# Optimization experiments

Hardware: AMD Instinct MI355X
Metric: run time of the kernel (lower is better)

The kernel has to match this reference:

```python
import jax, jax.numpy as jnp
import numpy as np

N_NODES = 100000


def setup_inputs() -> dict:
    key = jax.random.key(0)
    k1, k2, k3, k4, k5, k6 = jax.random.split(key, 6)
    N, E, DIN, DOUT = N_NODES, 1600000, 64, 64
    feature = jax.random.normal(k1, (N, DIN), dtype=jnp.float32)
    norm = jax.random.uniform(k2, (N, 1), dtype=jnp.float32)  # per-node 1/sqrt(deg)-style norm
    src = jax.random.randint(k3, (E,), 0, N, dtype=jnp.int32)
    dst = jax.random.randint(k4, (E,), 0, N, dtype=jnp.int32)
    W = jax.random.normal(k5, (DOUT, DIN), dtype=jnp.float32) / jnp.sqrt(jnp.float32(DIN))
    b = jax.random.normal(k6, (DOUT,), dtype=jnp.float32)
    return {"feature": feature, "norm": norm, "src": src, "dst": dst, "W": W, "b": b}


def reference(feature, norm, src, dst, W, b):
    # message: h_src * norm_src, gathered per edge -> [E, DIN]
    msg = (feature * norm)[src]
    # reduce: scatter-sum over destination nodes, then renormalize by dst norm
    accum = jax.ops.segment_sum(msg, dst, num_segments=N_NODES) * norm  # [N, DIN]
    # final Linear: accum @ W^T + b
    return accum @ W.T + b
```

## Files before the change

### kernel.cpp

```cpp
#include <hip/hip_runtime.h>
#include <hip/hip_bf16.h>

#define N_NODES 100000
#define D 64
#define BNODES 128
#define NBKT 782
#define SCAP 16
#define BCAP 4608
#define CAP 48
#define SENT 0xFFFFFFFFu

__global__ __launch_bounds__(256) void pre_linear_kernel(
    const float* __restrict__ feature,
    const float* __restrict__ norm,
    const float* __restrict__ W,
    __hip_bfloat16* __restrict__ Zb,
    int* __restrict__ bkt_cnt)
{
    __shared__ float Wt[D * 65];
    __shared__ float accsm[4][D];

    int gid = blockIdx.x * blockDim.x + threadIdx.x;
    if (gid < NBKT) bkt_cnt[gid] = 0;

    for (int i = threadIdx.x; i < D * D; i += blockDim.x) {
        int o = i >> 6, k = i & 63;
        Wt[k * 65 + o] = W[o * D + k];
    }
    __syncthreads();

    const int lane = threadIdx.x & 63;
    const int wid  = threadIdx.x >> 6;

    float wreg[D];
    #pragma unroll
    for (int k = 0; k < D; ++k) wreg[k] = Wt[k * 65 + lane];
    float* const mysm = &accsm[wid][0];

    const int wave   = gid >> 6;
    const int nwaves = gridDim.x * (blockDim.x >> 6);

    for (int node = wave; node < N_NODES; node += nwaves) {
        float x = feature[node * D + lane] * norm[node];
        mysm[lane] = x;
        __builtin_amdgcn_wave_barrier();
        float r = 0.f;
        #pragma unroll
        for (int j = 0; j < D / 4; ++j) {
            float4 a4 = *(const float4*)&mysm[j * 4];
            r = fmaf(a4.x, wreg[4 * j + 0], r);
            r = fmaf(a4.y, wreg[4 * j + 1], r);
            r = fmaf(a4.z, wreg[4 * j + 2], r);
            r = fmaf(a4.w, wreg[4 * j + 3], r);
        }
        Zb[node * D + lane] = __float2bfloat16(r);
        __builtin_amdgcn_wave_barrier();
    }
}

__global__ __launch_bounds__(1024) void bin_scatter_kernel(
    const int* __restrict__ src, const int* __restrict__ dst,
    int* __restrict__ bkt_cnt,
    unsigned int* __restrict__ barr,
    int E)
{
    __shared__ unsigned int stage[NBKT][SCAP];
    __shared__ int scnt[NBKT];

    for (int i = threadIdx.x; i < NBKT; i += blockDim.x) scnt[i] = 0;
    __syncthreads();

    const int nthreads = gridDim.x * blockDim.x;
    for (int e = blockIdx.x * blockDim.x + threadIdx.x; e < E; e += nthreads) {
        int t = dst[e];
        int b = t >> 7;
        unsigned u = ((unsigned)src[e] << 7) | (unsigned)(t & 127);
        int slot = atomicAdd(&scnt[b], 1);
        if (slot < SCAP) {
            stage[b][slot] = u;
        } else {
            int g = atomicAdd(&bkt_cnt[b], 16);
            if (g + 16 <= BCAP) {
                unsigned int* dp = barr + (size_t)b * BCAP + g;
                dp[0] = u;
                #pragma unroll
                for (int k = 1; k < 16; ++k) dp[k] = SENT;
            }
        }
    }
    __syncthreads();

    for (int bb = threadIdx.x; bb < NBKT; bb += blockDim.x) {
        int n_live = scnt[bb];
        if (n_live > SCAP) n_live = SCAP;
        if (n_live > 0) {
            int g = atomicAdd(&bkt_cnt[bb], 16);
            if (g + 16 <= BCAP) {
                unsigned int* dp = barr + (size_t)bb * BCAP + g;
                for (int k = 0; k < n_live; ++k) dp[k] = stage[bb][k];
                for (int k = n_live; k < 16; ++k) dp[k] = SENT;
            }
        }
    }
}

__device__ inline float2 bf2f(unsigned int z) {
    float2 r;
    r.x = __uint_as_float(z << 16);
    r.y = __uint_as_float(z & 0xffff0000u);
    return r;
}

__global__ __launch_bounds__(512) void csr_gather_kernel(
    const __hip_bfloat16* __restrict__ Zb,
    const float* __restrict__ norm,
    const int* __restrict__ bkt_cnt,
    const unsigned int* __restrict__ barr,
    const float* __restrict__ bias,
    float* __restrict__ out)
{
    __shared__ int slab[BNODES * CAP];
    __shared__ int lcnt[BNODES];

    const int b   = blockIdx.x;
    const int tid = threadIdx.x;

    for (int i = tid; i < BNODES; i += blockDim.x) lcnt[i] = 0;
    __syncthreads();

    int n = bkt_cnt[b];
    if (n > BCAP) n = BCAP;
    const unsigned int* bp = barr + (size_t)b * BCAP;
    for (int i = tid * 4; i < n; i += blockDim.x * 4) {
        uint4 u4 = *(const uint4*)&bp[i];
        unsigned us[4] = {u4.x, u4.y, u4.z, u4.w};
        #pragma unroll
        for (int j = 0; j < 4; ++j) {
            unsigned u = us[j];
            if (u != SENT) {
                int local = (int)(u & 127);
                int pos = atomicAdd(&lcnt[local], 1);
                if (pos < CAP) slab[local * CAP + pos] = (int)(u >> 7);
            }
        }
    }
    __syncthreads();

    const int lane = tid & 63;
    const int wid  = tid >> 6;
    const int q    = lane >> 4;
    const int c    = lane & 15;

    const float4 bi = *(const float4*)&bias[4 * c];

    for (int nl = wid; nl < BNODES; nl += 8) {
        int node = (b << 7) + nl;
        if (node >= N_NODES) continue;

        int len = lcnt[nl];
        if (len > CAP) len = CAP;
        const int* sl = &slab[nl * CAP];

        float ax = 0.f, ay = 0.f, az = 0.f, aw = 0.f;
        int i = 0;
        for (; i + 16 <= len; i += 16) {
            int s0 = sl[i + 0  + q];
            int s1 = sl[i + 4  + q];
            int s2 = sl[i + 8  + q];
            int s3 = sl[i + 12 + q];
            uint2 z0 = *(const uint2*)&Zb[s0 * D + 4 * c];
            uint2 z1 = *(const uint2*)&Zb[s1 * D + 4 * c];
            uint2 z2 = *(const uint2*)&Zb[s2 * D + 4 * c];
            uint2 z3 = *(const uint2*)&Zb[s3 * D + 4 * c];
            float2 a0 = bf2f(z0.x), b0 = bf2f(z0.y);
            float2 a1 = bf2f(z1.x), b1 = bf2f(z1.y);
            float2 a2 = bf2f(z2.x), b2 = bf2f(z2.y);
            float2 a3 = bf2f(z3.x), b3 = bf2f(z3.y);
            ax += a0.x + a1.x + a2.x + a3.x;
            ay += a0.y + a1.y + a2.y + a3.y;
            az += b0.x + b1.x + b2.x + b3.x;
            aw += b0.y + b1.y + b2.y + b3.y;
        }
        for (; i < len; i += 4) {
            int idx = i + q;
            if (idx < len) {
                int s = sl[idx];
                uint2 z = *(const uint2*)&Zb[s * D + 4 * c];
                float2 a = bf2f(z.x), bb2 = bf2f(z.y);
                ax += a.x; ay += a.y; az += bb2.x; aw += bb2.y;
            }
        }

        ax += __shfl(ax, lane ^ 16, 64);
        ay += __shfl(ay, lane ^ 16, 64);
        az += __shfl(az, lane ^ 16, 64);
        aw += __shfl(aw, lane ^ 16, 64);
        ax += __shfl(ax, lane ^ 32, 64);
        ay += __shfl(ay, lane ^ 32, 64);
        az += __shfl(az, lane ^ 32, 64);
        aw += __shfl(aw, lane ^ 32, 64);

        if (q == 0) {
            float nv = norm[node];
            float4 o;
            o.x = fmaf(nv, ax, bi.x);
            o.y = fmaf(nv, ay, bi.y);
            o.z = fmaf(nv, az, bi.z);
            o.w = fmaf(nv, aw, bi.w);
            *(float4*)&out[node * D + 4 * c] = o;
        }
    }
}

extern "C" void kernel_launch(void* const* d_in, const int* in_sizes, int n_in,
                              void* d_out, int out_size, void* d_ws, size_t ws_size,
                              hipStream_t stream)
{
    const float* feature = (const float*)d_in[0];
    const float* norm    = (const float*)d_in[1];
    const int*   src     = (const int*)d_in[2];
    const int*   dst     = (const int*)d_in[3];
    const float* W       = (const float*)d_in[4];
    const float* b       = (const float*)d_in[5];
    float*       out     = (float*)d_out;

    const int E = in_sizes[2];

    char* p = (char*)d_ws;
    __hip_bfloat16* Zb      = (__hip_bfloat16*)p;  p += (size_t)N_NODES * D * 2;
    unsigned int*   barr    = (unsigned int*)p;    p += (size_t)NBKT * BCAP * 4;
    int*            bkt_cnt = (int*)p;

    pre_linear_kernel<<<3125, 256, 0, stream>>>(feature, norm, W, Zb, bkt_cnt);

    bin_scatter_kernel<<<256, 1024, 0, stream>>>(src, dst, bkt_cnt, barr, E);

    csr_gather_kernel<<<NBKT, 512, 0, stream>>>(Zb, norm, bkt_cnt, barr, b, out);
}
```

Baseline: 169.3 us.

## Use fixed per-block bucket slots to drop global atomics in bin flush

Each of the 256 scatter blocks now writes its 16-entry staged chunk for every bucket into a fixed slot indexed by block and bucket, using vectorized uint4 stores from four threads per bucket. This removes the global atomicAdd on bkt_cnt during the flush phase; only overflow entries still go through atomics into a separate overflow region. The gather kernel reads all 256 fixed chunks per bucket plus the overflow region. In exchange it always writes and reads full sentinel-padded chunks even for empty buckets, which raises memory traffic and spreads each bucket's reads across strided addresses.

Result: faster. 159.7 us (-5.6%).

```diff
diff --git a/kernel.cpp b/kernel.cpp
--- a/kernel.cpp
+++ b/kernel.cpp
@@ -6,7 +6,9 @@
 #define BNODES 128
 #define NBKT 782
 #define SCAP 16
-#define BCAP 4608
+#define FIXU 256
+#define FIXED (FIXU * 16)
+#define OVCAP 1024
 #define CAP 48
 #define SENT 0xFFFFFFFFu
 
@@ -64,11 +66,13 @@
     unsigned int* __restrict__ barr,
     int E)
 {
-    __shared__ unsigned int stage[NBKT][SCAP];
+    __shared__ unsigned int stage[NBKT][17];
     __shared__ int scnt[NBKT];
 
     for (int i = threadIdx.x; i < NBKT; i += blockDim.x) scnt[i] = 0;
     __syncthreads();
+
+    unsigned int* const ov = barr + (size_t)NBKT * FIXED;
 
     const int nthreads = gridDim.x * blockDim.x;
     for (int e = blockIdx.x * blockDim.x + threadIdx.x; e < E; e += nthreads) {
@@ -80,8 +84,8 @@
             stage[b][slot] = u;
         } else {
             int g = atomicAdd(&bkt_cnt[b], 16);
-            if (g + 16 <= BCAP) {
-                unsigned int* dp = barr + (size_t)b * BCAP + g;
+            if (g + 16 <= OVCAP) {
+                unsigned int* dp = ov + (size_t)b * OVCAP + g;
                 dp[0] = u;
                 #pragma unroll
                 for (int k = 1; k < 16; ++k) dp[k] = SENT;
@@ -90,17 +94,17 @@
     }
     __syncthreads();
 
-    for (int bb = threadIdx.x; bb < NBKT; bb += blockDim.x) {
+    const size_t ubase = (size_t)blockIdx.x * NBKT;
+    for (int idx = threadIdx.x; idx < NBKT * 4; idx += blockDim.x) {
+        int bb = idx >> 2, j = idx & 3;
         int n_live = scnt[bb];
         if (n_live > SCAP) n_live = SCAP;
-        if (n_live > 0) {
-            int g = atomicAdd(&bkt_cnt[bb], 16);
-            if (g + 16 <= BCAP) {
-                unsigned int* dp = barr + (size_t)bb * BCAP + g;
-                for (int k = 0; k < n_live; ++k) dp[k] = stage[bb][k];
-                for (int k = n_live; k < 16; ++k) dp[k] = SENT;
-            }
-        }
+        int base = j * 4;
+        unsigned v0 = (base + 0 < n_live) ? stage[bb][base + 0] : SENT;
+        unsigned v1 = (base + 1 < n_live) ? stage[bb][base + 1] : SENT;
+        unsigned v2 = (base + 2 < n_live) ? stage[bb][base + 2] : SENT;
+        unsigned v3 = (base + 3 < n_live) ? stage[bb][base + 3] : SENT;
+        *(uint4*)&barr[(ubase + (size_t)bb) * 16 + base] = make_uint4(v0, v1, v2, v3);
     }
 }
 
@@ -128,19 +132,35 @@
     for (int i = tid; i < BNODES; i += blockDim.x) lcnt[i] = 0;
     __syncthreads();
 
-    int n = bkt_cnt[b];
-    if (n > BCAP) n = BCAP;
-    const unsigned int* bp = barr + (size_t)b * BCAP;
-    for (int i = tid * 4; i < n; i += blockDim.x * 4) {
-        uint4 u4 = *(const uint4*)&bp[i];
+    for (int idx = tid; idx < FIXU * 4; idx += blockDim.x) {
+        int bk = idx >> 2, j = idx & 3;
+        uint4 u4 = *(const uint4*)&barr[((size_t)bk * NBKT + (size_t)b) * 16 + j * 4];
         unsigned us[4] = {u4.x, u4.y, u4.z, u4.w};
         #pragma unroll
-        for (int j = 0; j < 4; ++j) {
-            unsigned u = us[j];
+        for (int k = 0; k < 4; ++k) {
+            unsigned u = us[k];
             if (u != SENT) {
                 int local = (int)(u & 127);
                 int pos = atomicAdd(&lcnt[local], 1);
                 if (pos < CAP) slab[local * CAP + pos] = (int)(u >> 7);
+            }
+        }
+    }
+    {
+        int n2 = bkt_cnt[b];
+        if (n2 > OVCAP) n2 = OVCAP;
+        const unsigned int* op = barr + (size_t)NBKT * FIXED + (size_t)b * OVCAP;
+        for (int i = tid * 4; i < n2; i += blockDim.x * 4) {
+            uint4 u4 = *(const uint4*)&op[i];
+            unsigned us[4] = {u4.x, u4.y, u4.z, u4.w};
+            #pragma unroll
+            for (int k = 0; k < 4; ++k) {
+                unsigned u = us[k];
+                if (u != SENT) {
+                    int local = (int)(u & 127);
+                    int pos = atomicAdd(&lcnt[local], 1);
+                    if (pos < CAP) slab[local * CAP + pos] = (int)(u >> 7);
+                }
             }
         }
     }
@@ -228,12 +248,12 @@
 
     char* p = (char*)d_ws;
     __hip_bfloat16* Zb      = (__hip_bfloat16*)p;  p += (size_t)N_NODES * D * 2;
-    unsigned int*   barr    = (unsigned int*)p;    p += (size_t)NBKT * BCAP * 4;
+    unsigned int*   barr    = (unsigned int*)p;    p += ((size_t)NBKT * FIXED + (size_t)NBKT * OVCAP) * 4;
     int*            bkt_cnt = (int*)p;
 
     pre_linear_kernel<<<3125, 256, 0, stream>>>(feature, norm, W, Zb, bkt_cnt);
 
-    bin_scatter_kernel<<<256, 1024, 0, stream>>>(src, dst, bkt_cnt, barr, E);
+    bin_scatter_kernel<<<FIXU, 1024, 0, stream>>>(src, dst, bkt_cnt, barr, E);
 
     csr_gather_kernel<<<NBKT, 512, 0, stream>>>(Zb, norm, bkt_cnt, barr, b, out);
 }
```
